# Kernel optimization log

Hardware: AMD Instinct MI355X
Metric: run time of the kernel (lower is better)

## Reference

```python
import jax, jax.numpy as jnp
import numpy as np

B, N, C, H = 16, 1024, 768, 12
HD = C // H  # head_dim = 64


def setup_inputs() -> dict:
    key = jax.random.key(0)
    ks = jax.random.split(key, 3)
    scale = 1.0 / np.sqrt(C)
    x = jax.random.normal(ks[0], (B, N, C), dtype=jnp.float32)
    Wqkv = jax.random.normal(ks[1], (C, 3 * C), dtype=jnp.float32) * scale
    bqkv = jnp.zeros((3 * C,), dtype=jnp.float32)
    Wout = jax.random.normal(ks[2], (C, C), dtype=jnp.float32) * scale
    bout = jnp.zeros((C,), dtype=jnp.float32)
    return {"x": x, "Wqkv": Wqkv, "bqkv": bqkv, "Wout": Wout, "bout": bout}


def reference(x, Wqkv, bqkv, Wout, bout):
    # QKV projection: [B,N,3C] -> [B,N,3,H,HD]
    qkv = (x @ Wqkv + bqkv).reshape(B, N, 3, H, HD)
    q = qkv[:, :, 0].transpose(0, 2, 1, 3)  # [B,H,N,HD]
    k = qkv[:, :, 1].transpose(0, 2, 1, 3)
    v = qkv[:, :, 2].transpose(0, 2, 1, 3)
    # Patch attention (the only path that reaches the output: the source's
    # cross-image attention result is overwritten before out_proj, so it is
    # dead code). Dropout is identity in eval mode.
    scores = jnp.einsum("bhqd,bhkd->bhqk", q, k) / np.sqrt(HD).astype(np.float32)
    attn = jax.nn.softmax(scores, axis=-1)
    out = jnp.einsum("bhqk,bhkd->bhqd", attn, v)  # [B,H,N,HD]
    out = out.transpose(0, 2, 1, 3).reshape(B, N, C)
    return out @ Wout + bout
```

## Files before the change

### kernel.cpp

```cpp
#include <hip/hip_runtime.h>
#include <hip/hip_bf16.h>

#define B_   16
#define N_   1024
#define C_   768
#define H_   12
#define HD_  64
#define M_   16384
#define N1_  2304
#define NEG_BIG (-1e30f)
#define LOG2E 1.4426950408889634f

typedef __attribute__((ext_vector_type(8))) _Float16 f16x8;
typedef __attribute__((ext_vector_type(4))) float f32x4;
typedef __attribute__((ext_vector_type(16))) float f32x16;

__device__ __forceinline__ unsigned short f2h(float f) {
  _Float16 h = (_Float16)f;
  union { _Float16 h; unsigned short u; } c; c.h = h; return c.u;
}
__device__ __forceinline__ unsigned int cvtpk_f16(float a, float b) {
  unsigned int r;
  asm("v_cvt_pkrtz_f16_f32 %0, %1, %2" : "=v"(r) : "v"(a), "v"(b));
  return r;
}
__device__ __forceinline__ float exp2_asm(float x) {
  float r;
  asm("v_exp_f32 %0, %1" : "=v"(r) : "v"(x));
  return r;
}

__device__ __forceinline__ void gload_lds16(const void* g, void* l) {
  __builtin_amdgcn_global_load_lds(
      (const __attribute__((address_space(1))) void*)g,
      (__attribute__((address_space(3))) void*)l, 16, 0, 0);
}

typedef __attribute__((ext_vector_type(8))) short u16x8;

__global__ __launch_bounds__(256)
void k_prep_all(const float* __restrict__ x, const float* __restrict__ Wqkv,
                const float* __restrict__ Wout,
                unsigned short* __restrict__ xh,
                unsigned short* __restrict__ WqkvT,
                unsigned short* __restrict__ WoutT) {
  int bid = blockIdx.x;
  if (bid < 6144) {
    long i = ((long)bid * 256 + threadIdx.x) * 8;
    float4 a = *(const float4*)(x + i);
    float4 b = *(const float4*)(x + i + 4);
    u16x8 v;
    v[0] = (short)f2h(a.x); v[1] = (short)f2h(a.y);
    v[2] = (short)f2h(a.z); v[3] = (short)f2h(a.w);
    v[4] = (short)f2h(b.x); v[5] = (short)f2h(b.y);
    v[6] = (short)f2h(b.z); v[7] = (short)f2h(b.w);
    *(u16x8*)(xh + i) = v;
  } else if (bid < 7008) {
    int tid = (bid - 6144) * 256 + threadIdx.x;
    int n  = tid % N1_;
    int kc = tid / N1_;
    u16x8 v;
#pragma unroll
    for (int j = 0; j < 8; ++j)
      v[j] = (short)f2h(Wqkv[(long)(kc * 8 + j) * N1_ + n]);
    *(u16x8*)(WqkvT + (long)n * C_ + kc * 8) = v;
  } else {
    int tid = (bid - 7008) * 256 + threadIdx.x;
    int n  = tid % C_;
    int kc = tid / C_;
    u16x8 v;
#pragma unroll
    for (int j = 0; j < 8; ++j)
      v[j] = (short)f2h(Wout[(long)(kc * 8 + j) * C_ + n]);
    *(u16x8*)(WoutT + (long)n * C_ + kc * 8) = v;
  }
}

__global__ __launch_bounds__(256) void k_transposeV2(const unsigned short* __restrict__ qkvb,
                                                     unsigned short* __restrict__ Vt) {
  __shared__ unsigned char lt[16384];
  int wid = (blockIdx.x & 7) * 192 + (blockIdx.x >> 3);
  int bh = wid >> 3, nb = wid & 7;
  int b = bh / H_, h = bh % H_;
  long tok0 = (long)b * N_ + nb * 128;
  int t = threadIdx.x;
  int d0 = (t & 7) * 8;
#pragma unroll
  for (int it = 0; it < 4; ++it) {
    int nl = it * 32 + (t >> 3);
    u16x8 v = *(const u16x8*)(qkvb + (tok0 + nl) * N1_ + 1536 + h * HD_ + d0);
#pragma unroll
    for (int j = 0; j < 8; ++j) {
      int d = d0 + j;
      *(unsigned short*)(lt + d * 256 + ((nl * 2) ^ (((d >> 3) & 7) << 4))) =
          (unsigned short)v[j];
    }
  }
  __syncthreads();
  int l = t & 63, wv = t >> 6;
  int p = l & 1;
  int dbase = ((l >> 1) & 7) * 8 + (l >> 4) * 2;
#pragma unroll
  for (int rr = 0; rr < 4; ++rr) {
    int d = dbase + (rr & 1);
    int n0 = wv * 32 + (rr >> 1) * 16 + p * 8;
    u16x8 v = *(const u16x8*)(lt + d * 256 + ((n0 * 2) ^ (((d >> 3) & 7) << 4)));
    *(u16x8*)(Vt + ((long)bh * HD_ + d) * N_ + nb * 128 + n0) = v;
  }
}

template <int STAGE>
__global__ __launch_bounds__(256, 4)
void gemm128(const unsigned short* __restrict__ A,
             const unsigned short* __restrict__ Bt,
             const float* __restrict__ bias,
             void* __restrict__ out, int Kdim, int Ndim) {
  __shared__ unsigned char lds[32768];
  const int t = threadIdx.x;
  const int l = t & 63, w = t >> 6;
  const int g = l >> 4, lr = l & 15;
  const int NB = Ndim >> 7;
  const int wgid = (blockIdx.x & 7) * (gridDim.x >> 3) + (blockIdx.x >> 3);
  const int mb = wgid / NB, nb = wgid % NB;
  const long m0 = (long)mb << 7, n0 = (long)nb << 7;
  const int wm = w >> 1, wn = w & 1;

  f32x4 acc[4][4];
  const f32x4 zz = {0.f, 0.f, 0.f, 0.f};
#pragma unroll
  for (int i = 0; i < 4; ++i)
#pragma unroll
    for (int j = 0; j < 4; ++j) acc[i][j] = zz;

  int srow[4], sx[4];
#pragma unroll
  for (int i = 0; i < 4; ++i) {
    int s = i * 4096 + t * 16;
    int row = s >> 7;
    srow[i] = row;
    sx[i] = (s & 127) ^ ((row & 7) << 4);
  }
  const char* Ab = (const char*)A;
  const char* Bb = (const char*)Bt;
  const long K2 = (long)Kdim * 2;
  const int wbase = (t & 192) * 16;

  for (int kt = 0; kt < Kdim; kt += 64) {
#pragma unroll
    for (int i = 0; i < 4; ++i) {
      const char* src = Ab + (m0 + srow[i]) * K2 + kt * 2 + sx[i];
      gload_lds16(src, (void*)(lds + i * 4096 + wbase));
    }
#pragma unroll
    for (int i = 0; i < 4; ++i) {
      const char* src = Bb + (n0 + srow[i]) * K2 + kt * 2 + sx[i];
      gload_lds16(src, (void*)(lds + 16384 + i * 4096 + wbase));
    }
    __syncthreads();
#pragma unroll
    for (int ks = 0; ks < 2; ++ks) {
      f16x8 af[4], bfr[4];
#pragma unroll
      for (int mi = 0; mi < 4; ++mi) {
        int row = wm * 64 + mi * 16 + lr;
        int off = row * 128 + ((ks * 64 + g * 16) ^ ((row & 7) << 4));
        af[mi] = *(const f16x8*)(lds + off);
      }
#pragma unroll
      for (int ni = 0; ni < 4; ++ni) {
        int row = wn * 64 + ni * 16 + lr;
        int off = 16384 + row * 128 + ((ks * 64 + g * 16) ^ ((row & 7) << 4));
        bfr[ni] = *(const f16x8*)(lds + off);
      }
#pragma unroll
      for (int mi = 0; mi < 4; ++mi)
#pragma unroll
        for (int ni = 0; ni < 4; ++ni)
          acc[mi][ni] = __builtin_amdgcn_mfma_f32_16x16x32_f16(
              af[mi], bfr[ni], acc[mi][ni], 0, 0, 0);
    }
    __syncthreads();
  }

  if (STAGE == 1) {
    float sc = (n0 < 768) ? 0.125f * LOG2E : 1.0f;
    unsigned short* cl = (unsigned short*)lds;
#pragma unroll
    for (int ni = 0; ni < 4; ++ni) {
      int col = wn * 64 + ni * 16 + lr;
      float bv = bias[(int)n0 + col];
#pragma unroll
      for (int mi = 0; mi < 4; ++mi)
#pragma unroll
        for (int r = 0; r < 4; ++r) {
          int row = wm * 64 + mi * 16 + g * 4 + r;
          cl[row * 128 + col] = f2h((acc[mi][ni][r] + bv) * sc);
        }
    }
    __syncthreads();
    unsigned short* o = (unsigned short*)out;
#pragma unroll
    for (int it = 0; it < 8; ++it) {
      int idx = it * 2048 + t * 8;
      int row = idx >> 7;
      int col = idx & 127;
      *(u16x8*)(o + (m0 + row) * N1_ + n0 + col) = *(const u16x8*)(cl + idx);
    }
  } else {
    float* o = (float*)out;
#pragma unroll
    for (int ni = 0; ni < 4; ++ni) {
      int col = (int)n0 + wn * 64 + ni * 16 + lr;
      float bv = bias[col];
#pragma unroll
      for (int mi = 0; mi < 4; ++mi)
#pragma unroll
        for (int r = 0; r < 4; ++r) {
          long rowm = m0 + wm * 64 + mi * 16 + g * 4 + r;
          o[rowm * C_ + col] = acc[mi][ni][r] + bv;
        }
    }
  }
}

__global__ __launch_bounds__(256, 4)
void attn_fused(const unsigned short* __restrict__ qkvb,
                const unsigned short* __restrict__ Vt,
                unsigned short* __restrict__ Ofp) {
  __shared__ unsigned char lds[32768];
  const int t = threadIdx.x, l = t & 63, w = t >> 6;
  const int q32 = l & 31;
  const int hi = l >> 5;
  const int hi16 = hi * 16;
  const int wid = (blockIdx.x & 7) * 192 + (blockIdx.x >> 3);
  const int bh = wid >> 3, qb = wid & 7;
  const int b = bh / H_, h = bh % H_;
  const long tok0 = (long)b * N_;
  const int q0 = qb * 128 + w * 32;
  const long mytok = tok0 + q0 + q32;

  f16x8 qa[4];
#pragma unroll
  for (int cs = 0; cs < 4; ++cs)
    qa[cs] = *(const f16x8*)(qkvb + mytok * N1_ + h * HD_ + cs * 16 + hi * 8);

  const f32x16 zz16 = {0.f};
  f32x16 o0 = zz16, o1 = zz16;
  f32x16 osum = zz16;
  float mrun = NEG_BIG;
  f16x8 ones;
#pragma unroll
  for (int i = 0; i < 8; ++i) ones[i] = (_Float16)1.0f;

  const int row0 = q32, row1 = 32 + q32;
  const int swz0 = (q32 & 7) << 4;

  const int sxs = ((t & 7) * 16) ^ (((t >> 3) & 7) << 4);
  const int wbase = (t & 192) * 16;
  const char* Vg = (const char*)(Vt + (long)bh * HD_ * N_);
  const char* Kg = (const char*)qkvb + ((tok0)*N1_ + C_ + h * HD_) * 2;

#define STAGE_KV(kv0, buf)                                                  \
  {                                                                         \
    _Pragma("unroll")                                                       \
    for (int i = 0; i < 2; ++i) {                                           \
      int row = i * 32 + (t >> 3);                                          \
      gload_lds16(Kg + ((long)(kv0 + row) * N1_) * 2 + sxs,                 \
                  (void*)((buf) + i * 4096 + wbase));                       \
    }                                                                       \
    _Pragma("unroll")                                                       \
    for (int i = 0; i < 2; ++i) {                                           \
      int row = i * 32 + (t >> 3);                                          \
      gload_lds16(Vg + ((long)row * N_ + (kv0)) * 2 + sxs,                  \
                  (void*)((buf) + 8192 + i * 4096 + wbase));                \
    }                                                                       \
  }

  STAGE_KV(0, lds);

#pragma unroll 2
  for (int tt = 0; tt < 16; ++tt) {
    unsigned char* curb = lds + (tt & 1) * 16384;
    unsigned char* nxtb = lds + ((tt & 1) ^ 1) * 16384;
    if (tt < 15) {
      STAGE_KV((tt + 1) * 64, nxtb);
      asm volatile("s_waitcnt vmcnt(4)" ::: "memory");
    } else {
      asm volatile("s_waitcnt vmcnt(0)" ::: "memory");
    }
    __builtin_amdgcn_s_barrier();
    __builtin_amdgcn_sched_barrier(0);

    f32x16 sa0 = zz16, sa1 = zz16;
#pragma unroll
    for (int cs = 0; cs < 4; ++cs) {
      f16x8 kf0 = *(const f16x8*)(curb + row0 * 128 + ((cs * 32 + hi16) ^ swz0));
      f16x8 kf1 = *(const f16x8*)(curb + row1 * 128 + ((cs * 32 + hi16) ^ swz0));
      sa0 = __builtin_amdgcn_mfma_f32_32x32x16_f16(kf0, qa[cs], sa0, 0, 0, 0);
      sa1 = __builtin_amdgcn_mfma_f32_32x32x16_f16(kf1, qa[cs], sa1, 0, 0, 0);
    }

    float tm[11];
#pragma unroll
    for (int i = 0; i < 5; ++i)
      tm[i] = fmaxf(fmaxf(sa0[3 * i], sa0[3 * i + 1]), sa0[3 * i + 2]);
    tm[5] = fmaxf(sa0[15], sa1[0]);
#pragma unroll
    for (int i = 0; i < 5; ++i)
      tm[6 + i] = fmaxf(fmaxf(sa1[3 * i + 1], sa1[3 * i + 2]), sa1[3 * i + 3]);
    float u0 = fmaxf(fmaxf(tm[0], tm[1]), tm[2]);
    float u1 = fmaxf(fmaxf(tm[3], tm[4]), tm[5]);
    float u2 = fmaxf(fmaxf(tm[6], tm[7]), tm[8]);
    float u3 = fmaxf(fmaxf(tm[9], tm[10]), u0);
    float mx = fmaxf(fmaxf(u1, u2), u3);
    mx = fmaxf(mx, __shfl_xor(mx, 32));
    if (!__all(mx <= mrun + 8.f)) {
      float mn = fmaxf(mrun, mx);
      float al = exp2_asm(mrun - mn);
      mrun = mn;
      o0 *= al;
      o1 *= al;
      osum[0] *= al;
    }
    float p0a[16], p1a[16];
#pragma unroll
    for (int i = 0; i < 16; ++i) p0a[i] = exp2_asm(sa0[i] - mrun);
#pragma unroll
    for (int i = 0; i < 16; ++i) p1a[i] = exp2_asm(sa1[i] - mrun);
    unsigned pk[2][4][2];
#pragma unroll
    for (int g = 0; g < 4; ++g) {
      pk[0][g][0] = cvtpk_f16(p0a[4 * g + 0], p0a[4 * g + 1]);
      pk[0][g][1] = cvtpk_f16(p0a[4 * g + 2], p0a[4 * g + 3]);
      pk[1][g][0] = cvtpk_f16(p1a[4 * g + 0], p1a[4 * g + 1]);
      pk[1][g][1] = cvtpk_f16(p1a[4 * g + 2], p1a[4 * g + 3]);
    }

    f16x8 pb[4];
#pragma unroll
    for (int tk = 0; tk < 2; ++tk)
#pragma unroll
      for (int par = 0; par < 2; ++par) {
        unsigned a0 = pk[tk][2 * par][0], b0 = pk[tk][2 * par + 1][0];
        unsigned a1 = pk[tk][2 * par][1], b1 = pk[tk][2 * par + 1][1];
        asm("v_permlane32_swap_b32 %0, %1" : "+v"(a0), "+v"(b0));
        asm("v_permlane32_swap_b32 %0, %1" : "+v"(a1), "+v"(b1));
        union { unsigned u[4]; f16x8 v; } pw;
        pw.u[0] = a0; pw.u[1] = a1; pw.u[2] = b0; pw.u[3] = b1;
        pb[2 * tk + par] = pw.v;
      }

#pragma unroll
    for (int kb = 0; kb < 4; ++kb) {
      f16x8 vf0 = *(const f16x8*)(curb + 8192 + row0 * 128 + ((kb * 32 + hi16) ^ swz0));
      f16x8 vf1 = *(const f16x8*)(curb + 8192 + row1 * 128 + ((kb * 32 + hi16) ^ swz0));
      o0 = __builtin_amdgcn_mfma_f32_32x32x16_f16(vf0, pb[kb], o0, 0, 0, 0);
      o1 = __builtin_amdgcn_mfma_f32_32x32x16_f16(vf1, pb[kb], o1, 0, 0, 0);
      osum = __builtin_amdgcn_mfma_f32_32x32x16_f16(ones, pb[kb], osum, 0, 0, 0);
    }
    __builtin_amdgcn_sched_barrier(0);
    asm volatile("s_waitcnt lgkmcnt(0)" ::: "memory");
    __builtin_amdgcn_s_barrier();
  }
#undef STAGE_KV

  float inv = 1.0f / osum[0];
  unsigned short* obase = Ofp + mytok * C_ + h * HD_;
#pragma unroll
  for (int dt = 0; dt < 2; ++dt) {
#pragma unroll
    for (int rp = 0; rp < 8; ++rp) {
      int r = rp * 2;
      float v0 = (dt ? o1[r] : o0[r]) * inv;
      float v1 = (dt ? o1[r + 1] : o0[r + 1]) * inv;
      unsigned hw = cvtpk_f16(v0, v1);
      int d = dt * 32 + (r & 3) + 8 * (r >> 2) + 4 * hi;
      *(unsigned*)(obase + d) = hw;
    }
  }
}

extern "C" void kernel_launch(void* const* d_in, const int* in_sizes, int n_in,
                              void* d_out, int out_size, void* d_ws, size_t ws_size,
                              hipStream_t stream) {
  const float* x    = (const float*)d_in[0];
  const float* Wqkv = (const float*)d_in[1];
  const float* bqkv = (const float*)d_in[2];
  const float* Wout = (const float*)d_in[3];
  const float* bout = (const float*)d_in[4];

  char* ws = (char*)d_ws;
  unsigned short* qkvb  = (unsigned short*)(ws);
  unsigned short* Ofp   = (unsigned short*)(ws + 75497472L);
  unsigned short* xh    = (unsigned short*)(ws + 100663296L);
  unsigned short* Vt    = (unsigned short*)(ws + 100663296L);
  unsigned short* WqkvT = (unsigned short*)(ws + 125829120L);
  unsigned short* WoutT = (unsigned short*)(ws + 129368064L);

  k_prep_all<<<7296, 256, 0, stream>>>(x, Wqkv, Wout, xh, WqkvT, WoutT);
  gemm128<1><<<2304, 256, 0, stream>>>(xh, WqkvT, bqkv, (void*)qkvb, 768, 2304);
  k_transposeV2<<<1536, 256, 0, stream>>>(qkvb, Vt);
  attn_fused<<<1536, 256, 0, stream>>>(qkvb, Vt, Ofp);
  gemm128<3><<<768, 256, 0, stream>>>(Ofp, WoutT, bout, d_out, 768, 768);
}
```

Baseline: 188.4 us.

## Fuse V transpose into QKV GEMM epilogue and compute softmax rowsum with VALU

The QKV GEMM blocks covering the V columns now write their tile transposed through LDS straight into the Vt layout, so the separate transpose kernel and its extra read and write of V are gone. Vt moves to its own workspace region because it no longer reuses the xh buffer after the GEMM. In attention, the row-sum MFMA with a ones vector is replaced by a VALU tree reduction plus a cross-half shuffle, and output stores are widened to 64-bit. The VALU sum adds ALU work inside the softmax loop in exchange for one fewer MFMA per k-block.

Result: faster. 177.9 us (-5.6%).

```diff
diff --git a/kernel.cpp b/kernel.cpp
--- a/kernel.cpp
+++ b/kernel.cpp
@@ -76,45 +76,13 @@
   }
 }
 
-__global__ __launch_bounds__(256) void k_transposeV2(const unsigned short* __restrict__ qkvb,
-                                                     unsigned short* __restrict__ Vt) {
-  __shared__ unsigned char lt[16384];
-  int wid = (blockIdx.x & 7) * 192 + (blockIdx.x >> 3);
-  int bh = wid >> 3, nb = wid & 7;
-  int b = bh / H_, h = bh % H_;
-  long tok0 = (long)b * N_ + nb * 128;
-  int t = threadIdx.x;
-  int d0 = (t & 7) * 8;
-#pragma unroll
-  for (int it = 0; it < 4; ++it) {
-    int nl = it * 32 + (t >> 3);
-    u16x8 v = *(const u16x8*)(qkvb + (tok0 + nl) * N1_ + 1536 + h * HD_ + d0);
-#pragma unroll
-    for (int j = 0; j < 8; ++j) {
-      int d = d0 + j;
-      *(unsigned short*)(lt + d * 256 + ((nl * 2) ^ (((d >> 3) & 7) << 4))) =
-          (unsigned short)v[j];
-    }
-  }
-  __syncthreads();
-  int l = t & 63, wv = t >> 6;
-  int p = l & 1;
-  int dbase = ((l >> 1) & 7) * 8 + (l >> 4) * 2;
-#pragma unroll
-  for (int rr = 0; rr < 4; ++rr) {
-    int d = dbase + (rr & 1);
-    int n0 = wv * 32 + (rr >> 1) * 16 + p * 8;
-    u16x8 v = *(const u16x8*)(lt + d * 256 + ((n0 * 2) ^ (((d >> 3) & 7) << 4)));
-    *(u16x8*)(Vt + ((long)bh * HD_ + d) * N_ + nb * 128 + n0) = v;
-  }
-}
-
 template <int STAGE>
 __global__ __launch_bounds__(256, 4)
 void gemm128(const unsigned short* __restrict__ A,
              const unsigned short* __restrict__ Bt,
              const float* __restrict__ bias,
-             void* __restrict__ out, int Kdim, int Ndim) {
+             void* __restrict__ out, unsigned short* __restrict__ Vt,
+             int Kdim, int Ndim) {
   __shared__ unsigned char lds[32768];
   const int t = threadIdx.x;
   const int l = t & 63, w = t >> 6;
@@ -182,7 +150,38 @@
     __syncthreads();
   }
 
-  if (STAGE == 1) {
+  if (STAGE == 1 && n0 >= 1536) {
+    unsigned short* lt = (unsigned short*)lds;
+#pragma unroll
+    for (int ni = 0; ni < 4; ++ni) {
+      int col = wn * 64 + ni * 16 + lr;
+      int s = (col & 15) << 3;
+      float bv = bias[(int)n0 + col];
+#pragma unroll
+      for (int mi = 0; mi < 4; ++mi) {
+        int rowb = wm * 64 + mi * 16 + g * 4;
+        unsigned d0 = cvtpk_f16(acc[mi][ni][0] + bv, acc[mi][ni][1] + bv);
+        unsigned d1 = cvtpk_f16(acc[mi][ni][2] + bv, acc[mi][ni][3] + bv);
+        unsigned long long dd = (unsigned long long)d0 |
+                                ((unsigned long long)d1 << 32);
+        *(unsigned long long*)(lt + col * 128 + (rowb ^ s)) = dd;
+      }
+    }
+    __syncthreads();
+    const int b_  = (int)(m0 >> 10);
+    const int nof = (int)(m0 & 1023);
+    const int h0  = ((int)n0 - 1536) >> 6;
+#pragma unroll
+    for (int it = 0; it < 8; ++it) {
+      int col  = it * 16 + (t >> 4);
+      int tokc = (t & 15) * 8;
+      int s = (col & 15) << 3;
+      u16x8 v = *(const u16x8*)(lt + col * 128 + (tokc ^ s));
+      int bh = b_ * H_ + h0 + (col >> 6);
+      int d  = col & 63;
+      *(u16x8*)(Vt + ((long)bh * HD_ + d) * N_ + nof + tokc) = v;
+    }
+  } else if (STAGE == 1) {
     float sc = (n0 < 768) ? 0.125f * LOG2E : 1.0f;
     unsigned short* cl = (unsigned short*)lds;
 #pragma unroll
@@ -246,11 +245,7 @@
 
   const f32x16 zz16 = {0.f};
   f32x16 o0 = zz16, o1 = zz16;
-  f32x16 osum = zz16;
-  float mrun = NEG_BIG;
-  f16x8 ones;
-#pragma unroll
-  for (int i = 0; i < 8; ++i) ones[i] = (_Float16)1.0f;
+  float mrun = NEG_BIG, lrun = 0.f;
 
   const int row0 = q32, row1 = 32 + q32;
   const int swz0 = (q32 & 7) << 4;
@@ -318,9 +313,9 @@
       float mn = fmaxf(mrun, mx);
       float al = exp2_asm(mrun - mn);
       mrun = mn;
+      lrun *= al;
       o0 *= al;
       o1 *= al;
-      osum[0] *= al;
     }
     float p0a[16], p1a[16];
 #pragma unroll
@@ -335,6 +330,16 @@
       pk[1][g][0] = cvtpk_f16(p1a[4 * g + 0], p1a[4 * g + 1]);
       pk[1][g][1] = cvtpk_f16(p1a[4 * g + 2], p1a[4 * g + 3]);
     }
+    float ts[16];
+#pragma unroll
+    for (int i = 0; i < 16; ++i) ts[i] = p0a[i] + p1a[i];
+#pragma unroll
+    for (int s = 8; s >= 1; s >>= 1)
+#pragma unroll
+      for (int i = 0; i < s; ++i) ts[i] += ts[i + s];
+    float rs = ts[0];
+    rs += __shfl_xor(rs, 32);
+    lrun += rs;
 
     f16x8 pb[4];
 #pragma unroll
@@ -356,7 +361,6 @@
       f16x8 vf1 = *(const f16x8*)(curb + 8192 + row1 * 128 + ((kb * 32 + hi16) ^ swz0));
       o0 = __builtin_amdgcn_mfma_f32_32x32x16_f16(vf0, pb[kb], o0, 0, 0, 0);
       o1 = __builtin_amdgcn_mfma_f32_32x32x16_f16(vf1, pb[kb], o1, 0, 0, 0);
-      osum = __builtin_amdgcn_mfma_f32_32x32x16_f16(ones, pb[kb], osum, 0, 0, 0);
     }
     __builtin_amdgcn_sched_barrier(0);
     asm volatile("s_waitcnt lgkmcnt(0)" ::: "memory");
@@ -364,18 +368,20 @@
   }
 #undef STAGE_KV
 
-  float inv = 1.0f / osum[0];
+  float inv = 1.0f / lrun;
   unsigned short* obase = Ofp + mytok * C_ + h * HD_;
 #pragma unroll
   for (int dt = 0; dt < 2; ++dt) {
 #pragma unroll
-    for (int rp = 0; rp < 8; ++rp) {
-      int r = rp * 2;
-      float v0 = (dt ? o1[r] : o0[r]) * inv;
-      float v1 = (dt ? o1[r + 1] : o0[r + 1]) * inv;
-      unsigned hw = cvtpk_f16(v0, v1);
-      int d = dt * 32 + (r & 3) + 8 * (r >> 2) + 4 * hi;
-      *(unsigned*)(obase + d) = hw;
+    for (int j = 0; j < 4; ++j) {
+      int r = 4 * j;
+      const f32x16& oo = dt ? o1 : o0;
+      unsigned hw0 = cvtpk_f16(oo[r] * inv, oo[r + 1] * inv);
+      unsigned hw1 = cvtpk_f16(oo[r + 2] * inv, oo[r + 3] * inv);
+      unsigned long long dd = (unsigned long long)hw0 |
+                              ((unsigned long long)hw1 << 32);
+      int d = dt * 32 + 8 * j + 4 * hi;
+      *(unsigned long long*)(obase + d) = dd;
     }
   }
 }
@@ -393,13 +399,12 @@
   unsigned short* qkvb  = (unsigned short*)(ws);
   unsigned short* Ofp   = (unsigned short*)(ws + 75497472L);
   unsigned short* xh    = (unsigned short*)(ws + 100663296L);
-  unsigned short* Vt    = (unsigned short*)(ws + 100663296L);
-  unsigned short* WqkvT = (unsigned short*)(ws + 125829120L);
-  unsigned short* WoutT = (unsigned short*)(ws + 129368064L);
+  unsigned short* Vt    = (unsigned short*)(ws + 125829120L);
+  unsigned short* WqkvT = (unsigned short*)(ws + 150994944L);
+  unsigned short* WoutT = (unsigned short*)(ws + 154533888L);
 
   k_prep_all<<<7296, 256, 0, stream>>>(x, Wqkv, Wout, xh, WqkvT, WoutT);
-  gemm128<1><<<2304, 256, 0, stream>>>(xh, WqkvT, bqkv, (void*)qkvb, 768, 2304);
-  k_transposeV2<<<1536, 256, 0, stream>>>(qkvb, Vt);
+  gemm128<1><<<2304, 256, 0, stream>>>(xh, WqkvT, bqkv, (void*)qkvb, Vt, 768, 2304);
   attn_fused<<<1536, 256, 0, stream>>>(qkvb, Vt, Ofp);
-  gemm128<3><<<768, 256, 0, stream>>>(Ofp, WoutT, bout, d_out, 768, 768);
-}
+  gemm128<3><<<768, 256, 0, stream>>>(Ofp, WoutT, bout, d_out, nullptr, 768, 768);
+}
```
